# Performance work log

Measured on AMD Instinct MI355X. Metric: run time of the kernel, lower is better.

Reference implementation:

```python
import jax, jax.numpy as jnp
import numpy as np

N, T, C, H = 32, 512, 768, 1536  # batch, seq_len, dim, int(dim*expand)


def setup_inputs() -> dict:
    key = jax.random.key(0)
    ks = jax.random.split(key, 10)
    sc = lambda fan: 1.0 / np.sqrt(fan)
    return {
        "x_seq": jax.random.normal(ks[0], (N, T, C), jnp.float32),
        "sup_seq": jax.random.uniform(ks[1], (N, T, 1), jnp.float32),
        # torch nn.Linear weights are [out, in]; y = x @ W.T + b
        "W_in": jax.random.normal(ks[2], (C, C), jnp.float32) * sc(C),
        "W_out": jax.random.normal(ks[3], (C, C), jnp.float32) * sc(C),
        "W_bg": jax.random.normal(ks[4], (C, C), jnp.float32) * sc(C),
        "b_bg": jax.random.normal(ks[5], (C,), jnp.float32) * 0.01,
        "W_sg": jax.random.normal(ks[6], (C, 1), jnp.float32),
        "b_sg": jax.random.normal(ks[7], (C,), jnp.float32) * 0.01,
        "W_f1": jax.random.normal(ks[8], (H, C), jnp.float32) * sc(C),
        "b_f1": jnp.zeros((H,), jnp.float32),
        "W_f2": jax.random.normal(ks[9], (C, H), jnp.float32) * sc(H),
        "b_f2": jnp.zeros((C,), jnp.float32),
    }


def reference(x_seq, sup_seq, W_in, W_out, W_bg, b_bg, W_sg, b_sg, W_f1, b_f1, W_f2, b_f2):
    # in_proj (no bias)
    x = jnp.einsum('ntc,dc->ntd', x_seq, W_in)                      # [N,T,C]
    # per-step FFN with residual (exact erf GELU, matching torch default)
    h = jax.nn.gelu(jnp.einsum('ntc,hc->nth', x, W_f1) + b_f1, approximate=False)
    xt = x + jnp.einsum('nth,ch->ntc', h, W_f2) + b_f2              # [N,T,C]
    # input-dependent gate (base_gate * sup_to_gate)
    g = jax.nn.sigmoid(jnp.einsum('ntc,dc->ntd', xt, W_bg) + b_bg)
    g = g * jax.nn.sigmoid(jnp.einsum('nto,do->ntd', sup_seq, W_sg) + b_sg)
    # linear recurrence s_t = (1-g_t)*s_{t-1} + g_t*xt_t, s_0 = 0 -> associative scan
    a = 1.0 - g
    b = g * xt

    def combine(c1, c2):
        a1, b1 = c1
        a2, b2 = c2
        return a2 * a1, a2 * b1 + b2

    _, s = jax.lax.associative_scan(combine, (a, b), axis=1)        # [N,T,C]
    return jnp.einsum('ntc,dc->ntd', s, W_out)
```

## Files before the change

kernel.cpp:

```cpp
#include <hip/hip_runtime.h>
#include <hip/hip_bf16.h>
#include <math.h>

typedef __bf16 bf16;
typedef __attribute__((ext_vector_type(8))) __bf16 bf16x8;
typedef __attribute__((ext_vector_type(4))) __bf16 bf16x4;
typedef __attribute__((ext_vector_type(4))) float f32x4;

constexpr int BM = 128, BN = 128, BK = 32;

enum { EPI_PLAIN = 0, EPI_GELU = 1, EPI_RES = 2, EPI_GATE = 3 };

__device__ __forceinline__ void async16(const void* g, void* l) {
  __builtin_amdgcn_global_load_lds(
      (const __attribute__((address_space(1))) void*)g,
      (__attribute__((address_space(3))) void*)l, 16, 0, 0);
}

__device__ __forceinline__ void bar_lgkm() {
  asm volatile("s_waitcnt lgkmcnt(0)\n\ts_barrier" ::: "memory");
}

#define WAIT_VM(n) asm volatile("s_waitcnt vmcnt(" #n ")" ::: "memory")

template <typename CT, int EPI>
__global__ __launch_bounds__(512, 4) void gemm_bt_a(
    const bf16* __restrict__ A, const bf16* __restrict__ B, CT* __restrict__ C,
    const float* __restrict__ bias, const bf16* __restrict__ resid,
    const float* __restrict__ sup, const float* __restrict__ wsg,
    const float* __restrict__ bsg, int M, int N, int K) {
  __shared__ bf16 As[2][BM * BK];
  __shared__ bf16 Bs[2][BN * BK];

  const int tid = threadIdx.x;
  const int nwg = gridDim.x;
  const int cpx = nwg >> 3;
  const int wg = blockIdx.x;
  const int sw = (wg & 7) * cpx + (wg >> 3);
  const int ntn = N >> 7;
  const int bm = sw / ntn, bn = sw - bm * ntn;

  const int lane = tid & 63;
  const int wv = tid >> 6;
  const int wm = (wv >> 2) * 64, wn = (wv & 3) * 32;
  const int quad = lane >> 4, l16 = lane & 15;

  f32x4 acc[4][2];
#pragma unroll
  for (int i = 0; i < 4; i++)
#pragma unroll
    for (int j = 0; j < 2; j++) acc[i][j] = f32x4{0.f, 0.f, 0.f, 0.f};

  const int srow = tid >> 2;
  const int sq8 = ((tid & 3) ^ ((srow >> 1) & 3)) * 8;
  const int slot8 = (quad ^ ((l16 >> 1) & 3)) * 8;

  const bf16* pa = A + (size_t)(bm * BM + srow) * K + sq8;
  const bf16* pb = B + (size_t)(bn * BN + srow) * K + sq8;
  bf16* dA = &As[0][0] + wv * 512;
  bf16* dB = &Bs[0][0] + wv * 512;

  auto stg = [&](int buf) {
    async16(pa, dA + buf * 4096);
    async16(pb, dB + buf * 4096);
    pa += BK;
    pb += BK;
  };

  stg(0);

  const int nt = K / BK;
  for (int t = 0; t < nt; ++t) {
    const int cur = t & 1;
    if (t + 1 < nt) {
      stg(cur ^ 1);
      WAIT_VM(2);
    } else {
      WAIT_VM(0);
    }
    bar_lgkm();

    bf16x8 af[4], bfr[2];
#pragma unroll
    for (int i = 0; i < 4; i++)
      af[i] = *(const bf16x8*)&As[cur][(wm + i * 16 + l16) * BK + slot8];
#pragma unroll
    for (int j = 0; j < 2; j++)
      bfr[j] = *(const bf16x8*)&Bs[cur][(wn + j * 16 + l16) * BK + slot8];
#pragma unroll
    for (int i = 0; i < 4; i++)
#pragma unroll
      for (int j = 0; j < 2; j++)
        acc[i][j] = __builtin_amdgcn_mfma_f32_16x16x32_bf16(af[i], bfr[j], acc[i][j], 0, 0, 0);
    bar_lgkm();
  }

#pragma unroll
  for (int i = 0; i < 4; i++) {
    int row0 = bm * BM + wm + i * 16 + quad * 4;
#pragma unroll
    for (int j = 0; j < 2; j++) {
      int col = bn * BN + wn + j * 16 + l16;
#pragma unroll
      for (int r = 0; r < 4; r++) {
        int row = row0 + r;
        size_t idx = (size_t)row * N + col;
        float v = acc[i][j][r];
        if constexpr (EPI == EPI_PLAIN) {
          C[idx] = (CT)v;
        } else if constexpr (EPI == EPI_GELU) {
          v += bias[col];
          float gl = 0.5f * v * (1.0f + erff(v * 0.70710678118654752f));
          C[idx] = (CT)gl;
        } else if constexpr (EPI == EPI_RES) {
          v += bias[col] + (float)resid[idx];
          C[idx] = (CT)v;
        } else {
          v += bias[col];
          float g1 = 1.0f / (1.0f + expf(-v));
          float z = sup[row] * wsg[col] + bsg[col];
          float g2 = 1.0f / (1.0f + expf(-z));
          C[idx] = (CT)(g1 * g2);
        }
      }
    }
  }
}

constexpr int SC_CH = 32, SC_NCH = 16, SC_CW = 32;

__global__ __launch_bounds__(512) void scan2_kernel(const float* __restrict__ g,
                                                    const bf16* __restrict__ xt,
                                                    bf16* __restrict__ s, int T, int C) {
  __shared__ float lA[SC_NCH][SC_CW];
  __shared__ float lB[SC_NCH][SC_CW];
  __shared__ float lC[SC_NCH][SC_CW];
  const int cl = threadIdx.x & (SC_CW - 1);
  const int ch = threadIdx.x / SC_CW;
  const int c = blockIdx.x * SC_CW + cl;
  const int n = blockIdx.y;
  const size_t base = ((size_t)n * T + ch * SC_CH) * C + c;

  float a_arr[SC_CH], sl[SC_CH];
  float A = 1.f, B = 0.f;
#pragma unroll
  for (int t = 0; t < SC_CH; ++t) {
    size_t idx = base + (size_t)t * C;
    float gv = g[idx], xv = (float)xt[idx];
    float at = 1.0f - gv;
    a_arr[t] = at;
    B = at * B + gv * xv;
    sl[t] = B;
    A *= at;
  }
  lA[ch][cl] = A;
  lB[ch][cl] = B;
  __syncthreads();
  if (ch == 0) {
    float carry = 0.f;
#pragma unroll
    for (int j = 0; j < SC_NCH; ++j) {
      lC[j][cl] = carry;
      carry = lA[j][cl] * carry + lB[j][cl];
    }
  }
  __syncthreads();
  const float carry = lC[ch][cl];
  float P = 1.f;
#pragma unroll
  for (int t = 0; t < SC_CH; ++t) {
    P *= a_arr[t];
    s[base + (size_t)t * C] = (bf16)(sl[t] + P * carry);
  }
}

__global__ __launch_bounds__(256) void cvt5_kernel(
    const float* s0, bf16* d0, int n0, const float* s1, bf16* d1, int n1,
    const float* s2, bf16* d2, int n2, const float* s3, bf16* d3, int n3,
    const float* s4, bf16* d4, int n4) {
  const float* s; bf16* d; int n;
  switch (blockIdx.y) {
    case 0: s = s0; d = d0; n = n0; break;
    case 1: s = s1; d = d1; n = n1; break;
    case 2: s = s2; d = d2; n = n2; break;
    case 3: s = s3; d = d3; n = n3; break;
    default: s = s4; d = d4; n = n4; break;
  }
  int i = blockIdx.x * 256 + threadIdx.x;
  if (i < n) d[i] = (bf16)s[i];
}

__global__ __launch_bounds__(256) void cvtx_kernel(const float* __restrict__ in,
                                                   bf16* __restrict__ out, int n4) {
  int i = blockIdx.x * 256 + threadIdx.x;
  if (i < n4) {
    f32x4 v = *(const f32x4*)(in + (size_t)i * 4);
    bf16x4 b;
    b[0] = (bf16)v[0]; b[1] = (bf16)v[1]; b[2] = (bf16)v[2]; b[3] = (bf16)v[3];
    *(bf16x4*)(out + (size_t)i * 4) = b;
  }
}

extern "C" void kernel_launch(void* const* d_in, const int* in_sizes, int n_in,
                              void* d_out, int out_size, void* d_ws, size_t ws_size,
                              hipStream_t stream) {
  const float* x_seq = (const float*)d_in[0];
  const float* sup = (const float*)d_in[1];
  const float* W_in = (const float*)d_in[2];
  const float* W_out = (const float*)d_in[3];
  const float* W_bg = (const float*)d_in[4];
  const float* b_bg = (const float*)d_in[5];
  const float* W_sg = (const float*)d_in[6];
  const float* b_sg = (const float*)d_in[7];
  const float* W_f1 = (const float*)d_in[8];
  const float* b_f1 = (const float*)d_in[9];
  const float* W_f2 = (const float*)d_in[10];
  const float* b_f2 = (const float*)d_in[11];

  const int Nb = 32, T = 512, C = 768, H = 1536;
  const int M = Nb * T;

  char* ws = (char*)d_ws;
  size_t off = 0;
  auto alloc = [&](size_t bytes) {
    void* p = ws + off;
    off += (bytes + 255) & ~(size_t)255;
    return p;
  };
  bf16* Win_bf = (bf16*)alloc((size_t)C * C * 2);
  bf16* Wf1_bf = (bf16*)alloc((size_t)H * C * 2);
  bf16* Wf2_bf = (bf16*)alloc((size_t)C * H * 2);
  bf16* Wbg_bf = (bf16*)alloc((size_t)C * C * 2);
  bf16* Wout_bf = (bf16*)alloc((size_t)C * C * 2);
  bf16* xs_bf = (bf16*)alloc((size_t)M * C * 2);
  bf16* x_bf = (bf16*)alloc((size_t)M * C * 2);
  bf16* h_bf = (bf16*)alloc((size_t)M * H * 2);
  bf16* xt_bf = (bf16*)alloc((size_t)M * C * 2);
  float* g_f = (float*)alloc((size_t)M * C * 4);
  bf16* s_bf = x_bf;

  cvt5_kernel<<<dim3((H * C + 255) / 256, 5), 256, 0, stream>>>(
      W_in, Win_bf, C * C, W_f1, Wf1_bf, H * C, W_f2, Wf2_bf, C * H,
      W_bg, Wbg_bf, C * C, W_out, Wout_bf, C * C);
  cvtx_kernel<<<(M * C / 4 + 255) / 256, 256, 0, stream>>>(x_seq, xs_bf, M * C / 4);

  dim3 blk(512);
  gemm_bt_a<bf16, EPI_PLAIN><<<dim3((M / BM) * (C / BN)), blk, 0, stream>>>(
      xs_bf, Win_bf, x_bf, nullptr, nullptr, nullptr, nullptr, nullptr, M, C, C);
  gemm_bt_a<bf16, EPI_GELU><<<dim3((M / BM) * (H / BN)), blk, 0, stream>>>(
      x_bf, Wf1_bf, h_bf, b_f1, nullptr, nullptr, nullptr, nullptr, M, H, C);
  gemm_bt_a<bf16, EPI_RES><<<dim3((M / BM) * (C / BN)), blk, 0, stream>>>(
      h_bf, Wf2_bf, xt_bf, b_f2, x_bf, nullptr, nullptr, nullptr, M, C, H);
  gemm_bt_a<float, EPI_GATE><<<dim3((M / BM) * (C / BN)), blk, 0, stream>>>(
      xt_bf, Wbg_bf, g_f, b_bg, nullptr, sup, W_sg, b_sg, M, C, C);
  scan2_kernel<<<dim3(C / SC_CW, Nb), dim3(SC_CW * SC_NCH), 0, stream>>>(
      g_f, xt_bf, s_bf, T, C);
  gemm_bt_a<float, EPI_PLAIN><<<dim3((M / BM) * (C / BN)), blk, 0, stream>>>(
      s_bf, Wout_bf, (float*)d_out, nullptr, nullptr, nullptr, nullptr, nullptr, M, C, C);
}
```

Before: 378.9 us.

## Fuse fp32 input conversion into in_proj GEMM and use 256-row tiles for FFN up-projection

Drops the separate fp32-to-bf16 conversion pass over x_seq. The in_proj GEMM now loads fp32 rows directly into registers, converts them and writes them to LDS, so the intermediate bf16 copy is never written or read back. The up-projection GEMM with GELU uses a 256x128 tile with a 4x4 MFMA fragment per wave to raise arithmetic intensity. All kernels move to launch bounds of 2 waves per SIMD. The fp32 path reads twice the bytes and uses synchronous loads, which may stall. The larger tile increases register pressure.

Measured after the change: 381.9 us. About the same (+0.8%).

```diff
diff --git a/kernel.cpp b/kernel.cpp
--- a/kernel.cpp
+++ b/kernel.cpp
@@ -7,8 +7,6 @@
 typedef __attribute__((ext_vector_type(4))) __bf16 bf16x4;
 typedef __attribute__((ext_vector_type(4))) float f32x4;
 
-constexpr int BM = 128, BN = 128, BK = 32;
-
 enum { EPI_PLAIN = 0, EPI_GELU = 1, EPI_RES = 2, EPI_GATE = 3 };
 
 __device__ __forceinline__ void async16(const void* g, void* l) {
@@ -22,15 +20,39 @@
 }
 
 #define WAIT_VM(n) asm volatile("s_waitcnt vmcnt(" #n ")" ::: "memory")
+#define MFMA16(d, va, vb) \
+  d = __builtin_amdgcn_mfma_f32_16x16x32_bf16(va, vb, d, 0, 0, 0)
 
 template <typename CT, int EPI>
-__global__ __launch_bounds__(512, 4) void gemm_bt_a(
+__device__ __forceinline__ void epi_store(
+    CT* C, size_t idx, float v, int row, int col, const float* bias,
+    const bf16* resid, const float* sup, const float* wsg, const float* bsg) {
+  if constexpr (EPI == EPI_PLAIN) {
+    C[idx] = (CT)v;
+  } else if constexpr (EPI == EPI_GELU) {
+    v += bias[col];
+    float gl = 0.5f * v * (1.0f + erff(v * 0.70710678118654752f));
+    C[idx] = (CT)gl;
+  } else if constexpr (EPI == EPI_RES) {
+    v += bias[col] + (float)resid[idx];
+    C[idx] = (CT)v;
+  } else {
+    v += bias[col];
+    float g1 = 1.0f / (1.0f + expf(-v));
+    float z = sup[row] * wsg[col] + bsg[col];
+    float g2 = 1.0f / (1.0f + expf(-z));
+    C[idx] = (CT)(g1 * g2);
+  }
+}
+
+template <typename CT, int EPI>
+__global__ __launch_bounds__(512, 2) void gemm256(
     const bf16* __restrict__ A, const bf16* __restrict__ B, CT* __restrict__ C,
     const float* __restrict__ bias, const bf16* __restrict__ resid,
     const float* __restrict__ sup, const float* __restrict__ wsg,
     const float* __restrict__ bsg, int M, int N, int K) {
-  __shared__ bf16 As[2][BM * BK];
-  __shared__ bf16 Bs[2][BN * BK];
+  __shared__ bf16 As[2][256 * 32];
+  __shared__ bf16 Bs[2][128 * 32];
 
   const int tid = threadIdx.x;
   const int nwg = gridDim.x;
@@ -42,86 +64,193 @@
 
   const int lane = tid & 63;
   const int wv = tid >> 6;
-  const int wm = (wv >> 2) * 64, wn = (wv & 3) * 32;
+  const int wm = (wv >> 1) * 64, wn = (wv & 1) * 64;
   const int quad = lane >> 4, l16 = lane & 15;
-
-  f32x4 acc[4][2];
+  const int slot8 = (quad ^ ((l16 >> 1) & 3)) * 8;
+
+  f32x4 acc[4][4];
 #pragma unroll
   for (int i = 0; i < 4; i++)
 #pragma unroll
-    for (int j = 0; j < 2; j++) acc[i][j] = f32x4{0.f, 0.f, 0.f, 0.f};
+    for (int j = 0; j < 4; j++) acc[i][j] = f32x4{0.f, 0.f, 0.f, 0.f};
 
   const int srow = tid >> 2;
   const int sq8 = ((tid & 3) ^ ((srow >> 1) & 3)) * 8;
-  const int slot8 = (quad ^ ((l16 >> 1) & 3)) * 8;
-
-  const bf16* pa = A + (size_t)(bm * BM + srow) * K + sq8;
-  const bf16* pb = B + (size_t)(bn * BN + srow) * K + sq8;
-  bf16* dA = &As[0][0] + wv * 512;
+  const bf16* pa0 = A + (size_t)(bm * 256 + srow) * K + sq8;
+  const bf16* pa1 = pa0 + (size_t)128 * K;
+  const bf16* pb = B + (size_t)(bn * 128 + srow) * K + sq8;
+  bf16* dA0 = &As[0][0] + wv * 512;
+  bf16* dA1 = &As[0][0] + 4096 + wv * 512;
   bf16* dB = &Bs[0][0] + wv * 512;
 
   auto stg = [&](int buf) {
-    async16(pa, dA + buf * 4096);
+    async16(pa0, dA0 + buf * 8192);
+    async16(pa1, dA1 + buf * 8192);
     async16(pb, dB + buf * 4096);
-    pa += BK;
-    pb += BK;
+    pa0 += 32; pa1 += 32; pb += 32;
   };
 
   stg(0);
 
-  const int nt = K / BK;
+  const int nt = K >> 5;
   for (int t = 0; t < nt; ++t) {
     const int cur = t & 1;
     if (t + 1 < nt) {
       stg(cur ^ 1);
-      WAIT_VM(2);
+      WAIT_VM(3);
     } else {
       WAIT_VM(0);
     }
     bar_lgkm();
 
+    bf16x8 af[4], bfr[4];
+#pragma unroll
+    for (int i = 0; i < 4; i++)
+      af[i] = *(const bf16x8*)&As[cur][(wm + i * 16 + l16) * 32 + slot8];
+#pragma unroll
+    for (int j = 0; j < 4; j++)
+      bfr[j] = *(const bf16x8*)&Bs[cur][(wn + j * 16 + l16) * 32 + slot8];
+#pragma unroll
+    for (int i = 0; i < 4; i++)
+#pragma unroll
+      for (int j = 0; j < 4; j++) MFMA16(acc[i][j], af[i], bfr[j]);
+    bar_lgkm();
+  }
+
+#pragma unroll
+  for (int i = 0; i < 4; i++) {
+    const int row0 = bm * 256 + wm + i * 16 + quad * 4;
+#pragma unroll
+    for (int j = 0; j < 4; j++) {
+      const int col = bn * 128 + wn + j * 16 + l16;
+#pragma unroll
+      for (int r = 0; r < 4; r++) {
+        const int row = row0 + r;
+        epi_store<CT, EPI>(C, (size_t)row * N + col, acc[i][j][r], row, col,
+                           bias, resid, sup, wsg, bsg);
+      }
+    }
+  }
+}
+
+template <typename CT, int EPI, int AFP32>
+__global__ __launch_bounds__(512, 2) void gemm128(
+    const bf16* __restrict__ A, const float* __restrict__ Af,
+    const bf16* __restrict__ B, CT* __restrict__ C,
+    const float* __restrict__ bias, const bf16* __restrict__ resid,
+    const float* __restrict__ sup, const float* __restrict__ wsg,
+    const float* __restrict__ bsg, int M, int N, int K) {
+  __shared__ bf16 As[2][128 * 32];
+  __shared__ bf16 Bs[2][128 * 32];
+
+  const int tid = threadIdx.x;
+  const int nwg = gridDim.x;
+  const int cpx = nwg >> 3;
+  const int wg = blockIdx.x;
+  const int sw = (wg & 7) * cpx + (wg >> 3);
+  const int ntn = N >> 7;
+  const int bm = sw / ntn, bn = sw - bm * ntn;
+
+  const int lane = tid & 63;
+  const int wv = tid >> 6;
+  const int wm = (wv >> 2) * 64, wn = (wv & 3) * 32;
+  const int quad = lane >> 4, l16 = lane & 15;
+  const int slot8 = (quad ^ ((l16 >> 1) & 3)) * 8;
+
+  f32x4 acc[4][2];
+#pragma unroll
+  for (int i = 0; i < 4; i++)
+#pragma unroll
+    for (int j = 0; j < 2; j++) acc[i][j] = f32x4{0.f, 0.f, 0.f, 0.f};
+
+  const int srow = tid >> 2;
+  const int sq8 = ((tid & 3) ^ ((srow >> 1) & 3)) * 8;
+  const bf16* pb = B + (size_t)(bn * 128 + srow) * K + sq8;
+  bf16* dB = &Bs[0][0] + wv * 512;
+
+  auto compute = [&](int buf) {
     bf16x8 af[4], bfr[2];
 #pragma unroll
     for (int i = 0; i < 4; i++)
-      af[i] = *(const bf16x8*)&As[cur][(wm + i * 16 + l16) * BK + slot8];
+      af[i] = *(const bf16x8*)&As[buf][(wm + i * 16 + l16) * 32 + slot8];
 #pragma unroll
     for (int j = 0; j < 2; j++)
-      bfr[j] = *(const bf16x8*)&Bs[cur][(wn + j * 16 + l16) * BK + slot8];
-#pragma unroll
-    for (int i = 0; i < 4; i++)
-#pragma unroll
-      for (int j = 0; j < 2; j++)
-        acc[i][j] = __builtin_amdgcn_mfma_f32_16x16x32_bf16(af[i], bfr[j], acc[i][j], 0, 0, 0);
-    bar_lgkm();
+      bfr[j] = *(const bf16x8*)&Bs[buf][(wn + j * 16 + l16) * 32 + slot8];
+#pragma unroll
+    for (int i = 0; i < 4; i++) {
+      MFMA16(acc[i][0], af[i], bfr[0]);
+      MFMA16(acc[i][1], af[i], bfr[1]);
+    }
+  };
+
+  const int nt = K >> 5;
+
+  if constexpr (!AFP32) {
+    const bf16* pa = A + (size_t)(bm * 128 + srow) * K + sq8;
+    bf16* dA = &As[0][0] + wv * 512;
+    auto stg = [&](int buf) {
+      async16(pa, dA + buf * 4096);
+      async16(pb, dB + buf * 4096);
+      pa += 32; pb += 32;
+    };
+    stg(0);
+    for (int t = 0; t < nt; ++t) {
+      const int cur = t & 1;
+      if (t + 1 < nt) {
+        stg(cur ^ 1);
+        WAIT_VM(2);
+      } else {
+        WAIT_VM(0);
+      }
+      bar_lgkm();
+      compute(cur);
+      bar_lgkm();
+    }
+  } else {
+    const float* pf = Af + (size_t)(bm * 128 + srow) * K + sq8;
+    bf16* wrA = &As[0][0] + tid * 8;
+    f32x4 fE0, fE1, fO0, fO1;
+
+    fE0 = *(const f32x4*)pf;
+    fE1 = *(const f32x4*)(pf + 4);
+    async16(pb, dB);
+
+    auto step = [&](int buf, f32x4& c0, f32x4& c1, f32x4& n0, f32x4& n1, int t) {
+      if (t + 1 < nt) {
+        const float* p = pf + (size_t)(t + 1) * 32;
+        n0 = *(const f32x4*)p;
+        n1 = *(const f32x4*)(p + 4);
+        async16(pb + (size_t)(t + 1) * 32, dB + (buf ^ 1) * 4096);
+        WAIT_VM(3);
+      } else {
+        WAIT_VM(0);
+      }
+      bf16x8 v;
+      v[0] = (bf16)c0[0]; v[1] = (bf16)c0[1]; v[2] = (bf16)c0[2]; v[3] = (bf16)c0[3];
+      v[4] = (bf16)c1[0]; v[5] = (bf16)c1[1]; v[6] = (bf16)c1[2]; v[7] = (bf16)c1[3];
+      *(bf16x8*)(wrA + buf * 4096) = v;
+      bar_lgkm();
+      compute(buf);
+      bar_lgkm();
+    };
+
+    for (int t = 0; t < nt; t += 2) {
+      step(0, fE0, fE1, fO0, fO1, t);
+      step(1, fO0, fO1, fE0, fE1, t + 1);
+    }
   }
 
 #pragma unroll
   for (int i = 0; i < 4; i++) {
-    int row0 = bm * BM + wm + i * 16 + quad * 4;
+    const int row0 = bm * 128 + wm + i * 16 + quad * 4;
 #pragma unroll
     for (int j = 0; j < 2; j++) {
-      int col = bn * BN + wn + j * 16 + l16;
+      const int col = bn * 128 + wn + j * 16 + l16;
 #pragma unroll
       for (int r = 0; r < 4; r++) {
-        int row = row0 + r;
-        size_t idx = (size_t)row * N + col;
-        float v = acc[i][j][r];
-        if constexpr (EPI == EPI_PLAIN) {
-          C[idx] = (CT)v;
-        } else if constexpr (EPI == EPI_GELU) {
-          v += bias[col];
-          float gl = 0.5f * v * (1.0f + erff(v * 0.70710678118654752f));
-          C[idx] = (CT)gl;
-        } else if constexpr (EPI == EPI_RES) {
-          v += bias[col] + (float)resid[idx];
-          C[idx] = (CT)v;
-        } else {
-          v += bias[col];
-          float g1 = 1.0f / (1.0f + expf(-v));
-          float z = sup[row] * wsg[col] + bsg[col];
-          float g2 = 1.0f / (1.0f + expf(-z));
-          C[idx] = (CT)(g1 * g2);
-        }
+        const int row = row0 + r;
+        epi_store<CT, EPI>(C, (size_t)row * N + col, acc[i][j][r], row, col,
+                           bias, resid, sup, wsg, bsg);
       }
     }
   }
@@ -188,17 +317,6 @@
   }
   int i = blockIdx.x * 256 + threadIdx.x;
   if (i < n) d[i] = (bf16)s[i];
-}
-
-__global__ __launch_bounds__(256) void cvtx_kernel(const float* __restrict__ in,
-                                                   bf16* __restrict__ out, int n4) {
-  int i = blockIdx.x * 256 + threadIdx.x;
-  if (i < n4) {
-    f32x4 v = *(const f32x4*)(in + (size_t)i * 4);
-    bf16x4 b;
-    b[0] = (bf16)v[0]; b[1] = (bf16)v[1]; b[2] = (bf16)v[2]; b[3] = (bf16)v[3];
-    *(bf16x4*)(out + (size_t)i * 4) = b;
-  }
 }
 
 extern "C" void kernel_launch(void* const* d_in, const int* in_sizes, int n_in,
@@ -232,7 +350,6 @@
   bf16* Wf2_bf = (bf16*)alloc((size_t)C * H * 2);
   bf16* Wbg_bf = (bf16*)alloc((size_t)C * C * 2);
   bf16* Wout_bf = (bf16*)alloc((size_t)C * C * 2);
-  bf16* xs_bf = (bf16*)alloc((size_t)M * C * 2);
   bf16* x_bf = (bf16*)alloc((size_t)M * C * 2);
   bf16* h_bf = (bf16*)alloc((size_t)M * H * 2);
   bf16* xt_bf = (bf16*)alloc((size_t)M * C * 2);
@@ -242,19 +359,18 @@
   cvt5_kernel<<<dim3((H * C + 255) / 256, 5), 256, 0, stream>>>(
       W_in, Win_bf, C * C, W_f1, Wf1_bf, H * C, W_f2, Wf2_bf, C * H,
       W_bg, Wbg_bf, C * C, W_out, Wout_bf, C * C);
-  cvtx_kernel<<<(M * C / 4 + 255) / 256, 256, 0, stream>>>(x_seq, xs_bf, M * C / 4);
 
   dim3 blk(512);
-  gemm_bt_a<bf16, EPI_PLAIN><<<dim3((M / BM) * (C / BN)), blk, 0, stream>>>(
-      xs_bf, Win_bf, x_bf, nullptr, nullptr, nullptr, nullptr, nullptr, M, C, C);
-  gemm_bt_a<bf16, EPI_GELU><<<dim3((M / BM) * (H / BN)), blk, 0, stream>>>(
+  gemm128<bf16, EPI_PLAIN, 1><<<dim3((M / 128) * (C / 128)), blk, 0, stream>>>(
+      nullptr, x_seq, Win_bf, x_bf, nullptr, nullptr, nullptr, nullptr, nullptr, M, C, C);
+  gemm256<bf16, EPI_GELU><<<dim3((M / 256) * (H / 128)), blk, 0, stream>>>(
       x_bf, Wf1_bf, h_bf, b_f1, nullptr, nullptr, nullptr, nullptr, M, H, C);
-  gemm_bt_a<bf16, EPI_RES><<<dim3((M / BM) * (C / BN)), blk, 0, stream>>>(
-      h_bf, Wf2_bf, xt_bf, b_f2, x_bf, nullptr, nullptr, nullptr, M, C, H);
-  gemm_bt_a<float, EPI_GATE><<<dim3((M / BM) * (C / BN)), blk, 0, stream>>>(
-      xt_bf, Wbg_bf, g_f, b_bg, nullptr, sup, W_sg, b_sg, M, C, C);
+  gemm128<bf16, EPI_RES, 0><<<dim3((M / 128) * (C / 128)), blk, 0, stream>>>(
+      h_bf, nullptr, Wf2_bf, xt_bf, b_f2, x_bf, nullptr, nullptr, nullptr, M, C, H);
+  gemm128<float, EPI_GATE, 0><<<dim3((M / 128) * (C / 128)), blk, 0, stream>>>(
+      xt_bf, nullptr, Wbg_bf, g_f, b_bg, nullptr, sup, W_sg, b_sg, M, C, C);
   scan2_kernel<<<dim3(C / SC_CW, Nb), dim3(SC_CW * SC_NCH), 0, stream>>>(
       g_f, xt_bf, s_bf, T, C);
-  gemm_bt_a<float, EPI_PLAIN><<<dim3((M / BM) * (C / BN)), blk, 0, stream>>>(
-      s_bf, Wout_bf, (float*)d_out, nullptr, nullptr, nullptr, nullptr, nullptr, M, C, C);
-}
+  gemm128<float, EPI_PLAIN, 0><<<dim3((M / 128) * (C / 128)), blk, 0, stream>>>(
+      s_bf, nullptr, Wout_bf, (float*)d_out, nullptr, nullptr, nullptr, nullptr, nullptr, M, C, C);
+}
```
